# Performance work log

Hardware: AMD Instinct MI355X
Metric: run time of the kernel (lower is better)

## Reference

```python
import jax, jax.numpy as jnp
import numpy as np

N = 262144  # number of points / sequence length
D = 64      # feature dim (qkv_dim); deterministic features => nb_features == D
KERNEL_EPSILON = 1e-3


def setup_inputs() -> dict:
    key = jax.random.key(0)
    ks = jax.random.split(key, 7)
    s = 1.0 / np.sqrt(D)
    return {
        "x": jax.random.normal(ks[0], (N, D), dtype=jnp.float32),
        "Wq": jax.random.normal(ks[1], (D, D), dtype=jnp.float32) * s,
        "bq": jnp.zeros((D,), dtype=jnp.float32),
        "Wk": jax.random.normal(ks[2], (D, D), dtype=jnp.float32) * s,
        "bk": jnp.zeros((D,), dtype=jnp.float32),
        "Wv": jax.random.normal(ks[3], (D, D), dtype=jnp.float32) * s,
        "bv": jnp.zeros((D,), dtype=jnp.float32),
    }


def reference(x, Wq, bq, Wk, bk, Wv, bv):
    # Dense projections (flax nn.Dense: x @ W + b)
    q = x @ Wq + bq  # [N, D]
    k = x @ Wk + bk
    v = x @ Wv + bv
    # Deterministic generalized kernel feature map: relu(data) + kernel_epsilon
    qp = jax.nn.relu(q) + KERNEL_EPSILON  # [N, M], M == D
    kp = jax.nn.relu(k) + KERNEL_EPSILON  # [N, M]
    # Bidirectional FAVOR+ linear attention: O(N*M*D)
    kv = jnp.einsum("nm,nd->md", kp, v)       # [M, D]
    num = jnp.einsum("nm,md->nd", qp, kv)     # [N, D]
    # renormalize_attention=True: divide by qp . sum(kp)
    denom = qp @ kp.sum(axis=0)               # [N]
    return num / denom[:, None]
```

## Files before the change

### kernel.cpp

```cpp
#include <hip/hip_runtime.h>
#include <hip/hip_bf16.h>


#define NPTS 262144
#define TILES (NPTS / 64)
#define GRID1 512
#define TPB1 (TILES / GRID1)
#define GRID2 1024
#define TPB2 (TILES / GRID2)
#define EPS 1e-3f

typedef __attribute__((ext_vector_type(8))) short short8;
typedef __attribute__((ext_vector_type(4))) float f32x4;

__device__ __forceinline__ unsigned short f2bf(float f) {
    unsigned u = __builtin_bit_cast(unsigned, f);
    u += 0x7FFFu + ((u >> 16) & 1u);
    return (unsigned short)(u >> 16);
}

__device__ __forceinline__ short8 cvt8(float4 p0, float4 p1) {
    short8 a;
    a[0] = (short)f2bf(p0.x); a[1] = (short)f2bf(p0.y); a[2] = (short)f2bf(p0.z); a[3] = (short)f2bf(p0.w);
    a[4] = (short)f2bf(p1.x); a[5] = (short)f2bf(p1.y); a[6] = (short)f2bf(p1.z); a[7] = (short)f2bf(p1.w);
    return a;
}

__device__ __forceinline__ void lds_barrier() {
    asm volatile("s_waitcnt lgkmcnt(0)" ::: "memory");
    __builtin_amdgcn_s_barrier();
}

__global__ __launch_bounds__(256, 2) void pass1_kernel(
    const float* __restrict__ x,
    const float* __restrict__ Wq, const float* __restrict__ bq,
    const float* __restrict__ Wk, const float* __restrict__ bk,
    const float* __restrict__ Wv, const float* __restrict__ bv,
    float* __restrict__ kvPart, float* __restrict__ ksPart,
    unsigned short* __restrict__ qpW)
{
    __shared__ unsigned short kpT[64][72];
    __shared__ unsigned short vT[64][72];
    __shared__ unsigned short qpT[64][72];
    __shared__ unsigned short wkF[8][64][8];
    __shared__ unsigned short wvF[8][64][8];
    __shared__ unsigned short wqF[8][64][8];

    const int tid = threadIdx.x;
    const int w = tid >> 6, l = tid & 63, l15 = l & 15, lg = l >> 4;

    {
        const float* Ws[3] = {Wk, Wv, Wq};
        unsigned short (*Fs[3])[64][8] = {wkF, wvF, wqF};
        const int srow = tid >> 2, sc0 = (tid & 3) * 16;
#pragma unroll
        for (int m = 0; m < 3; ++m) {
            const float* p = Ws[m] + srow * 64 + sc0;
            float4 f0 = ((const float4*)p)[0];
            float4 f1 = ((const float4*)p)[1];
            float4 f2 = ((const float4*)p)[2];
            float4 f3 = ((const float4*)p)[3];
            float ff[16] = {f0.x, f0.y, f0.z, f0.w, f1.x, f1.y, f1.z, f1.w,
                            f2.x, f2.y, f2.z, f2.w, f3.x, f3.y, f3.z, f3.w};
            unsigned hh[8];
#pragma unroll
            for (int e = 0; e < 8; ++e)
                hh[e] = (unsigned)f2bf(ff[2 * e]) | ((unsigned)f2bf(ff[2 * e + 1]) << 16);
            uint4 u0 = {hh[0], hh[1], hh[2], hh[3]};
            uint4 u1 = {hh[4], hh[5], hh[6], hh[7]};
            *(uint4*)&kpT[srow][sc0] = u0;
            *(uint4*)&kpT[srow][sc0 + 8] = u1;
            __syncthreads();
#pragma unroll
            for (int kk = 0; kk < 2; ++kk) {
                short8 t;
#pragma unroll
                for (int e = 0; e < 8; ++e)
                    t[e] = (short)kpT[kk * 32 + lg * 8 + e][w * 16 + l15];
                *(short8*)&Fs[m][w * 2 + kk][l][0] = t;
            }
            __syncthreads();
        }
    }
    float bkl[4], bvl[4], bql[4];
#pragma unroll
    for (int j = 0; j < 4; ++j) {
        bkl[j] = bk[j * 16 + l15]; bvl[j] = bv[j * 16 + l15]; bql[j] = bq[j * 16 + l15];
    }

    f32x4 akv[4];
#pragma unroll
    for (int j = 0; j < 4; ++j) akv[j] = (f32x4){0.f, 0.f, 0.f, 0.f};
    float ks[4] = {0.f, 0.f, 0.f, 0.f};

    const int t0 = blockIdx.x * TPB1;
    const float* xbase = x + ((size_t)t0 * 64 + w * 16 + l15) * 64 + lg * 8;
    float4 c0 = *(const float4*)(xbase + 0);
    float4 c1 = *(const float4*)(xbase + 4);
    float4 c2 = *(const float4*)(xbase + 32);
    float4 c3 = *(const float4*)(xbase + 36);
    const int nbase = w * 16 + lg * 4;

    for (int t = 0; t < TPB1; ++t) {
        const float* xn = xbase + (size_t)((t + 1 < TPB1) ? (t + 1) : t) * 4096;
        float4 n0 = *(const float4*)(xn + 0);
        float4 n1 = *(const float4*)(xn + 4);
        float4 n2 = *(const float4*)(xn + 32);
        float4 n3 = *(const float4*)(xn + 36);

        short8 a0 = cvt8(c0, c1);
        short8 a1 = cvt8(c2, c3);

#pragma unroll
        for (int j = 0; j < 4; ++j) {
            short8 bk0 = *(const short8*)&wkF[j * 2 + 0][l][0];
            short8 bk1 = *(const short8*)&wkF[j * 2 + 1][l][0];
            short8 bv0 = *(const short8*)&wvF[j * 2 + 0][l][0];
            short8 bv1 = *(const short8*)&wvF[j * 2 + 1][l][0];
            short8 bq0 = *(const short8*)&wqF[j * 2 + 0][l][0];
            short8 bq1 = *(const short8*)&wqF[j * 2 + 1][l][0];
            f32x4 z = (f32x4){0.f, 0.f, 0.f, 0.f};
            f32x4 ak = __builtin_amdgcn_mfma_f32_16x16x32_bf16(a0, bk0, z, 0, 0, 0);
            ak = __builtin_amdgcn_mfma_f32_16x16x32_bf16(a1, bk1, ak, 0, 0, 0);
            f32x4 av = __builtin_amdgcn_mfma_f32_16x16x32_bf16(a0, bv0, z, 0, 0, 0);
            av = __builtin_amdgcn_mfma_f32_16x16x32_bf16(a1, bv1, av, 0, 0, 0);
            f32x4 aq = __builtin_amdgcn_mfma_f32_16x16x32_bf16(a0, bq0, z, 0, 0, 0);
            aq = __builtin_amdgcn_mfma_f32_16x16x32_bf16(a1, bq1, aq, 0, 0, 0);
            unsigned short h[4], g[4], q[4];
#pragma unroll
            for (int r = 0; r < 4; ++r) {
                float kp = fmaxf(ak[r] + bkl[j], 0.f) + EPS;
                ks[j] += kp;
                h[r] = f2bf(kp);
                g[r] = f2bf(av[r] + bvl[j]);
                q[r] = f2bf(fmaxf(aq[r] + bql[j], 0.f) + EPS);
            }
            uint2 hp = {(unsigned)h[0] | ((unsigned)h[1] << 16), (unsigned)h[2] | ((unsigned)h[3] << 16)};
            uint2 gp = {(unsigned)g[0] | ((unsigned)g[1] << 16), (unsigned)g[2] | ((unsigned)g[3] << 16)};
            uint2 qp2 = {(unsigned)q[0] | ((unsigned)q[1] << 16), (unsigned)q[2] | ((unsigned)q[3] << 16)};
            *(uint2*)&kpT[j * 16 + l15][nbase] = hp;
            *(uint2*)&vT[j * 16 + l15][nbase] = gp;
            *(uint2*)&qpT[j * 16 + l15][nbase] = qp2;
        }
        lds_barrier();
        short8 ka0 = *(const short8*)&kpT[w * 16 + l15][lg * 8];
        short8 ka1 = *(const short8*)&kpT[w * 16 + l15][32 + lg * 8];
#pragma unroll
        for (int j = 0; j < 4; ++j) {
            short8 vb0 = *(const short8*)&vT[j * 16 + l15][lg * 8];
            short8 vb1 = *(const short8*)&vT[j * 16 + l15][32 + lg * 8];
            akv[j] = __builtin_amdgcn_mfma_f32_16x16x32_bf16(ka0, vb0, akv[j], 0, 0, 0);
            akv[j] = __builtin_amdgcn_mfma_f32_16x16x32_bf16(ka1, vb1, akv[j], 0, 0, 0);
        }
        short8 q0, q1;
#pragma unroll
        for (int e = 0; e < 8; ++e) {
            q0[e] = (short)qpT[lg * 8 + e][w * 16 + l15];
            q1[e] = (short)qpT[32 + lg * 8 + e][w * 16 + l15];
        }
        unsigned short* qdst = qpW + ((size_t)(t0 + t) * 64 + w * 16 + l15) * 64 + lg * 8;
        *(short8*)(qdst) = q0;
        *(short8*)(qdst + 32) = q1;
        lds_barrier();
        c0 = n0; c1 = n1; c2 = n2; c3 = n3;
    }

    float* kvs = kvPart + (size_t)blockIdx.x * 4096;
#pragma unroll
    for (int j = 0; j < 4; ++j)
#pragma unroll
        for (int r = 0; r < 4; ++r)
            kvs[(size_t)(w * 16 + lg * 4 + r) * 64 + j * 16 + l15] = akv[j][r];
#pragma unroll
    for (int j = 0; j < 4; ++j) {
        float s = ks[j];
        s += __shfl_xor(s, 16, 64);
        s += __shfl_xor(s, 32, 64);
        if (lg == 0) ksPart[(size_t)blockIdx.x * 256 + w * 64 + j * 16 + l15] = s;
    }
}

__global__ __launch_bounds__(256, 4) void reduce_kernel(
    const float* __restrict__ kvPart, const float* __restrict__ ksPart,
    float* __restrict__ kvFin, float* __restrict__ ksFin)
{
    __shared__ float red[4][64];
    const int b = blockIdx.x, t = threadIdx.x;
    const int oo = t & 63, sc = t >> 6;
    float acc = 0.f;
    if (b < 64) {
        const float* p = kvPart + (size_t)sc * 128 * 4096 + b * 64 + oo;
#pragma unroll 8
        for (int s = 0; s < GRID1 / 4; ++s) acc += p[(size_t)s * 4096];
    } else {
        const float* p = ksPart + (size_t)sc * GRID1 * 64 + oo;
#pragma unroll 8
        for (int s = 0; s < GRID1; ++s) acc += p[(size_t)s * 64];
    }
    red[sc][oo] = acc;
    __syncthreads();
    if (t < 64) {
        float s = red[0][t] + red[1][t] + red[2][t] + red[3][t];
        if (b < 64) kvFin[b * 64 + t] = s;
        else        ksFin[t] = s;
    }
}

__global__ __launch_bounds__(256, 4) void pass2_kernel(
    const unsigned short* __restrict__ qpW, const float* __restrict__ kvFin,
    const float* __restrict__ ksFin, float* __restrict__ out)
{
    __shared__ unsigned short kvS[64][72];

    const int tid = threadIdx.x;
    const int w = tid >> 6, l = tid & 63, l15 = l & 15, lg = l >> 4;

    {
        const int srow = tid >> 2, sc0 = (tid & 3) * 16;
        const float* p = kvFin + srow * 64 + sc0;
        float4 f0 = ((const float4*)p)[0];
        float4 f1 = ((const float4*)p)[1];
        float4 f2 = ((const float4*)p)[2];
        float4 f3 = ((const float4*)p)[3];
        float ff[16] = {f0.x, f0.y, f0.z, f0.w, f1.x, f1.y, f1.z, f1.w,
                        f2.x, f2.y, f2.z, f2.w, f3.x, f3.y, f3.z, f3.w};
        unsigned hh[8];
#pragma unroll
        for (int e = 0; e < 8; ++e)
            hh[e] = (unsigned)f2bf(ff[2 * e]) | ((unsigned)f2bf(ff[2 * e + 1]) << 16);
        uint4 u0 = {hh[0], hh[1], hh[2], hh[3]};
        uint4 u1 = {hh[4], hh[5], hh[6], hh[7]};
        *(uint4*)&kvS[srow][sc0] = u0;
        *(uint4*)&kvS[srow][sc0 + 8] = u1;
    }
    __syncthreads();
    short8 kvf[4][2];
#pragma unroll
    for (int j = 0; j < 4; ++j)
#pragma unroll
        for (int kk = 0; kk < 2; ++kk) {
            short8 t;
#pragma unroll
            for (int e = 0; e < 8; ++e)
                t[e] = (short)kvS[kk * 32 + lg * 8 + e][j * 16 + l15];
            kvf[j][kk] = t;
        }
    short8 ksf0, ksf1;
#pragma unroll
    for (int e = 0; e < 8; ++e) {
        ksf0[e] = (short)f2bf(ksFin[lg * 8 + e]);
        ksf1[e] = (short)f2bf(ksFin[32 + lg * 8 + e]);
    }

    const int t0 = blockIdx.x * TPB2;
    const unsigned short* qbase = qpW + ((size_t)t0 * 64 + w * 16 + l15) * 64 + lg * 8;
    short8 an0 = *(const short8*)(qbase);
    short8 an1 = *(const short8*)(qbase + 32);

#pragma unroll
    for (int t = 0; t < TPB2; ++t) {
        const unsigned short* qn = qbase + (size_t)((t + 1 < TPB2) ? (t + 1) : t) * 4096;
        short8 m0 = *(const short8*)(qn);
        short8 m1 = *(const short8*)(qn + 32);

        f32x4 z = (f32x4){0.f, 0.f, 0.f, 0.f};
        f32x4 dn = __builtin_amdgcn_mfma_f32_16x16x32_bf16(an0, ksf0, z, 0, 0, 0);
        dn = __builtin_amdgcn_mfma_f32_16x16x32_bf16(an1, ksf1, dn, 0, 0, 0);
        float inv[4];
#pragma unroll
        for (int r = 0; r < 4; ++r) inv[r] = __builtin_amdgcn_rcpf(dn[r]);

        const size_t row0 = (size_t)(t0 + t) * 64 + w * 16;
#pragma unroll
        for (int j = 0; j < 4; ++j) {
            f32x4 nm = __builtin_amdgcn_mfma_f32_16x16x32_bf16(an0, kvf[j][0], z, 0, 0, 0);
            nm = __builtin_amdgcn_mfma_f32_16x16x32_bf16(an1, kvf[j][1], nm, 0, 0, 0);
#pragma unroll
            for (int r = 0; r < 4; ++r)
                out[(row0 + lg * 4 + r) * 64 + j * 16 + l15] = nm[r] * inv[r];
        }
        an0 = m0; an1 = m1;
    }
}

extern "C" void kernel_launch(void* const* d_in, const int* in_sizes, int n_in,
                              void* d_out, int out_size, void* d_ws, size_t ws_size,
                              hipStream_t stream)
{
    const float* x  = (const float*)d_in[0];
    const float* Wq = (const float*)d_in[1];
    const float* bq = (const float*)d_in[2];
    const float* Wk = (const float*)d_in[3];
    const float* bk = (const float*)d_in[4];
    const float* Wv = (const float*)d_in[5];
    const float* bv = (const float*)d_in[6];
    float* out = (float*)d_out;

    float* kvPart = (float*)d_ws;
    float* ksPart = kvPart + (size_t)GRID1 * 4096;
    float* kvFin  = ksPart + (size_t)GRID1 * 256;
    float* ksFin  = kvFin + 4096;
    unsigned short* qpW = (unsigned short*)(ksFin + 64);

    hipLaunchKernelGGL(pass1_kernel, dim3(GRID1), dim3(256), 0, stream,
                       x, Wq, bq, Wk, bk, Wv, bv, kvPart, ksPart, qpW);
    hipLaunchKernelGGL(reduce_kernel, dim3(65), dim3(256), 0, stream,
                       kvPart, ksPart, kvFin, ksFin);
    hipLaunchKernelGGL(pass2_kernel, dim3(GRID2), dim3(256), 0, stream,
                       qpW, kvFin, ksFin, out);
}
```

Baseline: 64.61 us.

## Recompute Q projection in pass2 from x instead of staging qp buffer

Pass1 no longer computes or writes the bf16 qp intermediate. Pass2 re-reads x and recomputes q = relu(xWq+bq)+eps on the fly with MFMA, computing the denominator in fp32 with a shuffle reduction. Operand order is swapped so each lane stores four contiguous output floats. Pass1's grid doubles with higher occupancy, and the reduce kernel is reshaped to match. The aim is to remove the qp write and read round trip, relying on the second read of x hitting in cache, at the cost of extra projection MFMAs in pass2.

```diff
diff --git a/kernel.cpp b/kernel.cpp
--- a/kernel.cpp
+++ b/kernel.cpp
@@ -4,7 +4,7 @@
 
 #define NPTS 262144
 #define TILES (NPTS / 64)
-#define GRID1 512
+#define GRID1 1024
 #define TPB1 (TILES / GRID1)
 #define GRID2 1024
 #define TPB2 (TILES / GRID2)
@@ -31,30 +31,26 @@
     __builtin_amdgcn_s_barrier();
 }
 
-__global__ __launch_bounds__(256, 2) void pass1_kernel(
+__global__ __launch_bounds__(256, 4) void pass1_kernel(
     const float* __restrict__ x,
-    const float* __restrict__ Wq, const float* __restrict__ bq,
     const float* __restrict__ Wk, const float* __restrict__ bk,
     const float* __restrict__ Wv, const float* __restrict__ bv,
-    float* __restrict__ kvPart, float* __restrict__ ksPart,
-    unsigned short* __restrict__ qpW)
+    float* __restrict__ kvPart, float* __restrict__ ksPart)
 {
     __shared__ unsigned short kpT[64][72];
     __shared__ unsigned short vT[64][72];
-    __shared__ unsigned short qpT[64][72];
     __shared__ unsigned short wkF[8][64][8];
     __shared__ unsigned short wvF[8][64][8];
-    __shared__ unsigned short wqF[8][64][8];
 
     const int tid = threadIdx.x;
     const int w = tid >> 6, l = tid & 63, l15 = l & 15, lg = l >> 4;
 
     {
-        const float* Ws[3] = {Wk, Wv, Wq};
-        unsigned short (*Fs[3])[64][8] = {wkF, wvF, wqF};
+        const float* Ws[2] = {Wk, Wv};
+        unsigned short (*Fs[2])[64][8] = {wkF, wvF};
         const int srow = tid >> 2, sc0 = (tid & 3) * 16;
 #pragma unroll
-        for (int m = 0; m < 3; ++m) {
+        for (int m = 0; m < 2; ++m) {
             const float* p = Ws[m] + srow * 64 + sc0;
             float4 f0 = ((const float4*)p)[0];
             float4 f1 = ((const float4*)p)[1];
@@ -82,11 +78,9 @@
             __syncthreads();
         }
     }
-    float bkl[4], bvl[4], bql[4];
-#pragma unroll
-    for (int j = 0; j < 4; ++j) {
-        bkl[j] = bk[j * 16 + l15]; bvl[j] = bv[j * 16 + l15]; bql[j] = bq[j * 16 + l15];
-    }
+    float bkl[4], bvl[4];
+#pragma unroll
+    for (int j = 0; j < 4; ++j) { bkl[j] = bk[j * 16 + l15]; bvl[j] = bv[j * 16 + l15]; }
 
     f32x4 akv[4];
 #pragma unroll
@@ -101,6 +95,7 @@
     float4 c3 = *(const float4*)(xbase + 36);
     const int nbase = w * 16 + lg * 4;
 
+#pragma unroll
     for (int t = 0; t < TPB1; ++t) {
         const float* xn = xbase + (size_t)((t + 1 < TPB1) ? (t + 1) : t) * 4096;
         float4 n0 = *(const float4*)(xn + 0);
@@ -117,30 +112,23 @@
             short8 bk1 = *(const short8*)&wkF[j * 2 + 1][l][0];
             short8 bv0 = *(const short8*)&wvF[j * 2 + 0][l][0];
             short8 bv1 = *(const short8*)&wvF[j * 2 + 1][l][0];
-            short8 bq0 = *(const short8*)&wqF[j * 2 + 0][l][0];
-            short8 bq1 = *(const short8*)&wqF[j * 2 + 1][l][0];
             f32x4 z = (f32x4){0.f, 0.f, 0.f, 0.f};
             f32x4 ak = __builtin_amdgcn_mfma_f32_16x16x32_bf16(a0, bk0, z, 0, 0, 0);
             ak = __builtin_amdgcn_mfma_f32_16x16x32_bf16(a1, bk1, ak, 0, 0, 0);
             f32x4 av = __builtin_amdgcn_mfma_f32_16x16x32_bf16(a0, bv0, z, 0, 0, 0);
             av = __builtin_amdgcn_mfma_f32_16x16x32_bf16(a1, bv1, av, 0, 0, 0);
-            f32x4 aq = __builtin_amdgcn_mfma_f32_16x16x32_bf16(a0, bq0, z, 0, 0, 0);
-            aq = __builtin_amdgcn_mfma_f32_16x16x32_bf16(a1, bq1, aq, 0, 0, 0);
-            unsigned short h[4], g[4], q[4];
+            unsigned short h[4], g[4];
 #pragma unroll
             for (int r = 0; r < 4; ++r) {
                 float kp = fmaxf(ak[r] + bkl[j], 0.f) + EPS;
                 ks[j] += kp;
                 h[r] = f2bf(kp);
                 g[r] = f2bf(av[r] + bvl[j]);
-                q[r] = f2bf(fmaxf(aq[r] + bql[j], 0.f) + EPS);
             }
             uint2 hp = {(unsigned)h[0] | ((unsigned)h[1] << 16), (unsigned)h[2] | ((unsigned)h[3] << 16)};
             uint2 gp = {(unsigned)g[0] | ((unsigned)g[1] << 16), (unsigned)g[2] | ((unsigned)g[3] << 16)};
-            uint2 qp2 = {(unsigned)q[0] | ((unsigned)q[1] << 16), (unsigned)q[2] | ((unsigned)q[3] << 16)};
             *(uint2*)&kpT[j * 16 + l15][nbase] = hp;
             *(uint2*)&vT[j * 16 + l15][nbase] = gp;
-            *(uint2*)&qpT[j * 16 + l15][nbase] = qp2;
         }
         lds_barrier();
         short8 ka0 = *(const short8*)&kpT[w * 16 + l15][lg * 8];
@@ -152,15 +140,6 @@
             akv[j] = __builtin_amdgcn_mfma_f32_16x16x32_bf16(ka0, vb0, akv[j], 0, 0, 0);
             akv[j] = __builtin_amdgcn_mfma_f32_16x16x32_bf16(ka1, vb1, akv[j], 0, 0, 0);
         }
-        short8 q0, q1;
-#pragma unroll
-        for (int e = 0; e < 8; ++e) {
-            q0[e] = (short)qpT[lg * 8 + e][w * 16 + l15];
-            q1[e] = (short)qpT[32 + lg * 8 + e][w * 16 + l15];
-        }
-        unsigned short* qdst = qpW + ((size_t)(t0 + t) * 64 + w * 16 + l15) * 64 + lg * 8;
-        *(short8*)(qdst) = q0;
-        *(short8*)(qdst + 32) = q1;
         lds_barrier();
         c0 = n0; c1 = n1; c2 = n2; c3 = n3;
     }
@@ -184,39 +163,82 @@
     const float* __restrict__ kvPart, const float* __restrict__ ksPart,
     float* __restrict__ kvFin, float* __restrict__ ksFin)
 {
-    __shared__ float red[4][64];
+    __shared__ float red[256];
     const int b = blockIdx.x, t = threadIdx.x;
-    const int oo = t & 63, sc = t >> 6;
-    float acc = 0.f;
-    if (b < 64) {
-        const float* p = kvPart + (size_t)sc * 128 * 4096 + b * 64 + oo;
-#pragma unroll 8
-        for (int s = 0; s < GRID1 / 4; ++s) acc += p[(size_t)s * 4096];
+    if (b < 128) {
+        const int o = b * 32 + (t & 31), sc = t >> 5;
+        float a0 = 0.f, a1 = 0.f;
+        const float* p = kvPart + (size_t)sc * 128 * 4096 + o;
+#pragma unroll 4
+        for (int s = 0; s < 128; s += 2) {
+            a0 += p[(size_t)s * 4096];
+            a1 += p[(size_t)(s + 1) * 4096];
+        }
+        red[sc * 32 + (t & 31)] = a0 + a1;
+        __syncthreads();
+        if (t < 32) {
+            float s = 0.f;
+#pragma unroll
+            for (int i = 0; i < 8; ++i) s += red[i * 32 + t];
+            kvFin[b * 32 + t] = s;
+        }
     } else {
-        const float* p = ksPart + (size_t)sc * GRID1 * 64 + oo;
-#pragma unroll 8
-        for (int s = 0; s < GRID1; ++s) acc += p[(size_t)s * 64];
-    }
-    red[sc][oo] = acc;
-    __syncthreads();
-    if (t < 64) {
-        float s = red[0][t] + red[1][t] + red[2][t] + red[3][t];
-        if (b < 64) kvFin[b * 64 + t] = s;
-        else        ksFin[t] = s;
+        const int oo = t & 63, sc = t >> 6;
+        float a0 = 0.f, a1 = 0.f;
+        const float* p = ksPart + (size_t)sc * 1024 * 64 + oo;
+#pragma unroll 4
+        for (int s = 0; s < 1024; s += 2) {
+            a0 += p[(size_t)s * 64];
+            a1 += p[(size_t)(s + 1) * 64];
+        }
+        red[sc * 64 + oo] = a0 + a1;
+        __syncthreads();
+        if (t < 64) ksFin[t] = red[t] + red[64 + t] + red[128 + t] + red[192 + t];
     }
 }
 
 __global__ __launch_bounds__(256, 4) void pass2_kernel(
-    const unsigned short* __restrict__ qpW, const float* __restrict__ kvFin,
-    const float* __restrict__ ksFin, float* __restrict__ out)
+    const float* __restrict__ x, const float* __restrict__ Wq, const float* __restrict__ bq,
+    const float* __restrict__ kvFin, const float* __restrict__ ksFin,
+    float* __restrict__ out)
 {
-    __shared__ unsigned short kvS[64][72];
+    __shared__ unsigned short stageS[64][72];
+    __shared__ unsigned short wqF[8][64][8];
 
     const int tid = threadIdx.x;
     const int w = tid >> 6, l = tid & 63, l15 = l & 15, lg = l >> 4;
+    const int srow = tid >> 2, sc0 = (tid & 3) * 16;
 
     {
-        const int srow = tid >> 2, sc0 = (tid & 3) * 16;
+        const float* p = Wq + srow * 64 + sc0;
+        float4 f0 = ((const float4*)p)[0];
+        float4 f1 = ((const float4*)p)[1];
+        float4 f2 = ((const float4*)p)[2];
+        float4 f3 = ((const float4*)p)[3];
+        float ff[16] = {f0.x, f0.y, f0.z, f0.w, f1.x, f1.y, f1.z, f1.w,
+                        f2.x, f2.y, f2.z, f2.w, f3.x, f3.y, f3.z, f3.w};
+        unsigned hh[8];
+#pragma unroll
+        for (int e = 0; e < 8; ++e)
+            hh[e] = (unsigned)f2bf(ff[2 * e]) | ((unsigned)f2bf(ff[2 * e + 1]) << 16);
+        uint4 u0 = {hh[0], hh[1], hh[2], hh[3]};
+        uint4 u1 = {hh[4], hh[5], hh[6], hh[7]};
+        *(uint4*)&stageS[srow][sc0] = u0;
+        *(uint4*)&stageS[srow][sc0 + 8] = u1;
+    }
+    __syncthreads();
+    {
+#pragma unroll
+        for (int kk = 0; kk < 2; ++kk) {
+            short8 t;
+#pragma unroll
+            for (int e = 0; e < 8; ++e)
+                t[e] = (short)stageS[kk * 32 + lg * 8 + e][w * 16 + l15];
+            *(short8*)&wqF[w * 2 + kk][l][0] = t;
+        }
+    }
+    __syncthreads();
+    {
         const float* p = kvFin + srow * 64 + sc0;
         float4 f0 = ((const float4*)p)[0];
         float4 f1 = ((const float4*)p)[1];
@@ -230,56 +252,81 @@
             hh[e] = (unsigned)f2bf(ff[2 * e]) | ((unsigned)f2bf(ff[2 * e + 1]) << 16);
         uint4 u0 = {hh[0], hh[1], hh[2], hh[3]};
         uint4 u1 = {hh[4], hh[5], hh[6], hh[7]};
-        *(uint4*)&kvS[srow][sc0] = u0;
-        *(uint4*)&kvS[srow][sc0 + 8] = u1;
+        *(uint4*)&stageS[srow][sc0] = u0;
+        *(uint4*)&stageS[srow][sc0 + 8] = u1;
     }
     __syncthreads();
-    short8 kvf[4][2];
-#pragma unroll
-    for (int j = 0; j < 4; ++j)
+    short8 kvA[4][2];
+#pragma unroll
+    for (int dj = 0; dj < 4; ++dj)
 #pragma unroll
         for (int kk = 0; kk < 2; ++kk) {
             short8 t;
 #pragma unroll
-            for (int e = 0; e < 8; ++e)
-                t[e] = (short)kvS[kk * 32 + lg * 8 + e][j * 16 + l15];
-            kvf[j][kk] = t;
-        }
-    short8 ksf0, ksf1;
-#pragma unroll
-    for (int e = 0; e < 8; ++e) {
-        ksf0[e] = (short)f2bf(ksFin[lg * 8 + e]);
-        ksf1[e] = (short)f2bf(ksFin[32 + lg * 8 + e]);
-    }
+            for (int e = 0; e < 8; ++e) {
+                int m = (kk * 2 + (e >> 2)) * 16 + lg * 4 + (e & 3);
+                t[e] = (short)stageS[m][dj * 16 + l15];
+            }
+            kvA[dj][kk] = t;
+        }
+    float bql2[4][4], ksl2[4][4];
+#pragma unroll
+    for (int jm = 0; jm < 4; ++jm)
+#pragma unroll
+        for (int r = 0; r < 4; ++r) {
+            bql2[jm][r] = bq[jm * 16 + lg * 4 + r];
+            ksl2[jm][r] = ksFin[jm * 16 + lg * 4 + r];
+        }
 
     const int t0 = blockIdx.x * TPB2;
-    const unsigned short* qbase = qpW + ((size_t)t0 * 64 + w * 16 + l15) * 64 + lg * 8;
-    short8 an0 = *(const short8*)(qbase);
-    short8 an1 = *(const short8*)(qbase + 32);
+    const float* xbase = x + ((size_t)t0 * 64 + w * 16 + l15) * 64 + lg * 8;
+    float4 c0 = *(const float4*)(xbase + 0);
+    float4 c1 = *(const float4*)(xbase + 4);
+    float4 c2 = *(const float4*)(xbase + 32);
+    float4 c3 = *(const float4*)(xbase + 36);
 
 #pragma unroll
     for (int t = 0; t < TPB2; ++t) {
-        const unsigned short* qn = qbase + (size_t)((t + 1 < TPB2) ? (t + 1) : t) * 4096;
-        short8 m0 = *(const short8*)(qn);
-        short8 m1 = *(const short8*)(qn + 32);
-
-        f32x4 z = (f32x4){0.f, 0.f, 0.f, 0.f};
-        f32x4 dn = __builtin_amdgcn_mfma_f32_16x16x32_bf16(an0, ksf0, z, 0, 0, 0);
-        dn = __builtin_amdgcn_mfma_f32_16x16x32_bf16(an1, ksf1, dn, 0, 0, 0);
-        float inv[4];
-#pragma unroll
-        for (int r = 0; r < 4; ++r) inv[r] = __builtin_amdgcn_rcpf(dn[r]);
-
-        const size_t row0 = (size_t)(t0 + t) * 64 + w * 16;
-#pragma unroll
-        for (int j = 0; j < 4; ++j) {
-            f32x4 nm = __builtin_amdgcn_mfma_f32_16x16x32_bf16(an0, kvf[j][0], z, 0, 0, 0);
-            nm = __builtin_amdgcn_mfma_f32_16x16x32_bf16(an1, kvf[j][1], nm, 0, 0, 0);
-#pragma unroll
-            for (int r = 0; r < 4; ++r)
-                out[(row0 + lg * 4 + r) * 64 + j * 16 + l15] = nm[r] * inv[r];
-        }
-        an0 = m0; an1 = m1;
+        const float* xn = xbase + (size_t)((t + 1 < TPB2) ? (t + 1) : t) * 4096;
+        float4 n0 = *(const float4*)(xn + 0);
+        float4 n1 = *(const float4*)(xn + 4);
+        float4 n2 = *(const float4*)(xn + 32);
+        float4 n3 = *(const float4*)(xn + 36);
+
+        short8 a0 = cvt8(c0, c1);
+        short8 a1 = cvt8(c2, c3);
+
+        const f32x4 z = (f32x4){0.f, 0.f, 0.f, 0.f};
+        float dp = 0.f;
+        short8 qb0, qb1;
+#pragma unroll
+        for (int jm = 0; jm < 4; ++jm) {
+            short8 wq0 = *(const short8*)&wqF[jm * 2 + 0][l][0];
+            short8 wq1 = *(const short8*)&wqF[jm * 2 + 1][l][0];
+            f32x4 aq = __builtin_amdgcn_mfma_f32_16x16x32_bf16(wq0, a0, z, 0, 0, 0);
+            aq = __builtin_amdgcn_mfma_f32_16x16x32_bf16(wq1, a1, aq, 0, 0, 0);
+#pragma unroll
+            for (int r = 0; r < 4; ++r) {
+                float qv = fmaxf(aq[r] + bql2[jm][r], 0.f) + EPS;
+                dp += qv * ksl2[jm][r];
+                unsigned short h = f2bf(qv);
+                if (jm < 2) qb0[(jm & 1) * 4 + r] = (short)h;
+                else        qb1[(jm & 1) * 4 + r] = (short)h;
+            }
+        }
+        dp += __shfl_xor(dp, 16, 64);
+        dp += __shfl_xor(dp, 32, 64);
+        const float inv = __builtin_amdgcn_rcpf(dp);
+
+        const size_t nrow = (size_t)(t0 + t) * 64 + w * 16 + l15;
+#pragma unroll
+        for (int dj = 0; dj < 4; ++dj) {
+            f32x4 nm = __builtin_amdgcn_mfma_f32_16x16x32_bf16(kvA[dj][0], qb0, z, 0, 0, 0);
+            nm = __builtin_amdgcn_mfma_f32_16x16x32_bf16(kvA[dj][1], qb1, nm, 0, 0, 0);
+            f32x4 o4 = {nm[0] * inv, nm[1] * inv, nm[2] * inv, nm[3] * inv};
+            *(f32x4*)(out + nrow * 64 + dj * 16 + lg * 4) = o4;
+        }
+        c0 = n0; c1 = n1; c2 = n2; c3 = n3;
     }
 }
 
@@ -300,12 +347,11 @@
     float* ksPart = kvPart + (size_t)GRID1 * 4096;
     float* kvFin  = ksPart + (size_t)GRID1 * 256;
     float* ksFin  = kvFin + 4096;
-    unsigned short* qpW = (unsigned short*)(ksFin + 64);
 
     hipLaunchKernelGGL(pass1_kernel, dim3(GRID1), dim3(256), 0, stream,
-                       x, Wq, bq, Wk, bk, Wv, bv, kvPart, ksPart, qpW);
-    hipLaunchKernelGGL(reduce_kernel, dim3(65), dim3(256), 0, stream,
+                       x, Wk, bk, Wv, bv, kvPart, ksPart);
+    hipLaunchKernelGGL(reduce_kernel, dim3(129), dim3(256), 0, stream,
                        kvPart, ksPart, kvFin, ksFin);
     hipLaunchKernelGGL(pass2_kernel, dim3(GRID2), dim3(256), 0, stream,
-                       qpW, kvFin, ksFin, out);
-}
+                       x, Wq, bq, kvFin, ksFin, out);
+}
```

Result: slower. 84.97 us (+31.5%).
